# Kernel tuning notes

Hardware: AMD Instinct MI355X
Metric: run time of the kernel (lower is better)

The kernel has to match this reference:

```python
import jax, jax.numpy as jnp
import numpy as np
import math

N_HEADS = 16
KV_HEADS = 4
HEAD_DIM = 128
ROPE_BASE = 1000000.0


def _make_rope(seq_len, dim, base=ROPE_BASE):
    inv_freq = 1.0 / (base ** (np.arange(0, dim, 2, dtype=np.float32) / dim))
    t = np.arange(seq_len, dtype=np.float32)
    freqs = np.outer(t, inv_freq)                     # [S, dim/2]
    emb = np.concatenate([freqs, freqs], axis=-1)     # [S, dim]
    return jnp.asarray(np.cos(emb)), jnp.asarray(np.sin(emb))


def setup_inputs() -> dict:
    key = jax.random.key(0)
    ks = jax.random.split(key, 6)
    B, S, H = 2, 2048, 2048
    kv_dim = KV_HEADS * HEAD_DIM
    s = 1.0 / math.sqrt(H)
    x = jax.random.normal(ks[0], (B, S, H), jnp.float32)
    wq = jax.random.normal(ks[1], (H, H), jnp.float32) * s
    wk = jax.random.normal(ks[2], (kv_dim, H), jnp.float32) * s
    wv = jax.random.normal(ks[3], (kv_dim, H), jnp.float32) * s
    wo = jax.random.normal(ks[4], (H, H), jnp.float32) * s
    bq = jnp.zeros((H,), jnp.float32)
    bk = jnp.zeros((kv_dim,), jnp.float32)
    bv = jnp.zeros((kv_dim,), jnp.float32)
    bo = jnp.zeros((H,), jnp.float32)
    cos, sin = _make_rope(S, HEAD_DIM)
    return {"x": x, "wq": wq, "bq": bq, "wk": wk, "bk": bk,
            "wv": wv, "bv": bv, "wo": wo, "bo": bo, "cos": cos, "sin": sin}


def _rotate_half(t):
    half = t.shape[-1] // 2
    return jnp.concatenate([-t[..., half:], t[..., :half]], axis=-1)


def reference(x, wq, bq, wk, bk, wv, bv, wo, bo, cos, sin):
    B, S, H = x.shape
    hd, nh, kvh = HEAD_DIM, N_HEADS, KV_HEADS
    rep = nh // kvh

    q = (x @ wq.T + bq).reshape(B, S, nh, hd)
    k = (x @ wk.T + bk).reshape(B, S, kvh, hd)
    v = (x @ wv.T + bv).reshape(B, S, kvh, hd)

    # RoPE (rotate-half), cos/sin: [S, hd] -> broadcast over batch and heads
    c = cos[None, :, None, :]
    s_ = sin[None, :, None, :]
    q = q * c + _rotate_half(q) * s_
    k = k * c + _rotate_half(k) * s_

    # GQA: expand KV heads by rep
    k = jnp.repeat(k, rep, axis=2)   # [B, S, nh, hd]
    v = jnp.repeat(v, rep, axis=2)

    q = q.transpose(0, 2, 1, 3)      # [B, nh, S, hd]
    k = k.transpose(0, 2, 1, 3)
    v = v.transpose(0, 2, 1, 3)

    score = jnp.einsum('bhqd,bhkd->bhqk', q, k) / math.sqrt(hd)
    causal = jnp.triu(jnp.full((S, S), -jnp.inf, jnp.float32), k=1)
    score = score + causal
    attn = jax.nn.softmax(score.astype(jnp.float32), axis=-1).astype(q.dtype)

    out = jnp.einsum('bhqk,bhkd->bhqd', attn, v)   # [B, nh, S, hd]
    out = out.transpose(0, 2, 1, 3).reshape(B, S, nh * hd)
    return out @ wo.T + bo
```

## Files before the change

### kernel.cpp

```cpp
#include <hip/hip_runtime.h>

typedef unsigned short u16;
typedef __bf16 bf16x8 __attribute__((ext_vector_type(8)));
typedef float  f32x4  __attribute__((ext_vector_type(4)));

#define SEQ 2048

__device__ __forceinline__ float bf2f(u16 u) {
    union { unsigned int i; float f; } c;
    c.i = ((unsigned int)u) << 16;
    return c.f;
}
__device__ __forceinline__ u16 f2bf(float f) {
    union { float f; unsigned int i; } c;
    c.f = f;
    unsigned int u = c.i;
    u += 0x7FFFu + ((u >> 16) & 1u);
    return (u16)(u >> 16);
}

__device__ __forceinline__ void gl_lds16(const u16* g, u16* l) {
    __builtin_amdgcn_global_load_lds(
        (const __attribute__((address_space(1))) unsigned int*)(g),
        (__attribute__((address_space(3))) unsigned int*)(l), 16, 0, 0);
}

__device__ __forceinline__ void cvt4(const float* s, u16* d) {
    float4 v = *(const float4*)s;
    ushort4 o;
    o.x = f2bf(v.x); o.y = f2bf(v.y); o.z = f2bf(v.z); o.w = f2bf(v.w);
    *(ushort4*)d = o;
}

__global__ void prep(const float* __restrict__ x,
                     const float* __restrict__ wq, const float* __restrict__ wk,
                     const float* __restrict__ wv,
                     const float* __restrict__ bq, const float* __restrict__ bk,
                     const float* __restrict__ bv,
                     u16* __restrict__ xb, u16* __restrict__ wqkvb,
                     float* __restrict__ biasb)
{
    const int E0 = 2097152;
    const int E1 = E0 + 1048576;
    const int E2 = E1 + 262144;
    const int E3 = E2 + 262144;
    const int E4 = E3 + 768;
    int i = blockIdx.x * blockDim.x + threadIdx.x;
    int stride = gridDim.x * blockDim.x;
    for (; i < E4; i += stride) {
        if (i < E0)      cvt4(x  + (size_t)i * 4,        xb    + (size_t)i * 4);
        else if (i < E1) cvt4(wq + (size_t)(i - E0) * 4, wqkvb + (size_t)(i - E0) * 4);
        else if (i < E2) cvt4(wk + (size_t)(i - E1) * 4, wqkvb + 4194304 + (size_t)(i - E1) * 4);
        else if (i < E3) cvt4(wv + (size_t)(i - E2) * 4, wqkvb + 5242880 + (size_t)(i - E2) * 4);
        else {
            int j = i - E3;
            const float* src = (j < 512) ? (bq + j * 4)
                             : (j < 640) ? (bk + (j - 512) * 4)
                                         : (bv + (j - 640) * 4);
            *(float4*)&biasb[j * 4] = *(const float4*)src;
        }
    }
}

__global__ void cvt_f32_bf16(const float* __restrict__ in, u16* __restrict__ out, int n4) {
    int i = blockIdx.x * blockDim.x + threadIdx.x;
    int stride = gridDim.x * blockDim.x;
    for (; i < n4; i += stride) cvt4(in + (size_t)i * 4, out + (size_t)i * 4);
}

template<int MODE>
__global__ __launch_bounds__(256) void gemm_bt(
    const u16* __restrict__ A, const u16* __restrict__ B,
    const float* __restrict__ bias, float* __restrict__ C,
    u16* __restrict__ qb, u16* __restrict__ kb, u16* __restrict__ vt,
    int M, int N, int K)
{
    __shared__ __align__(16) u16 lA[128 * 32];
    __shared__ __align__(16) u16 lB[128 * 32];
    const int tid   = threadIdx.x;
    const int lane  = tid & 63;
    const int wave  = tid >> 6;
    const int waveM = (wave >> 1) * 64;
    const int waveN = (wave & 1) * 64;
    const int bm = blockIdx.x * 128;
    const int bn = blockIdx.y * 128;
    const int lrow = lane & 15;
    const int koff = (lane >> 4) * 8;

    f32x4 acc[4][4] = {};

    for (int k0 = 0; k0 < K; k0 += 32) {
        __syncthreads();
#pragma unroll
        for (int p = 0; p < 2; ++p) {
            int idx = p * 256 + tid;
            int row = idx >> 2;
            int ch  = idx & 3;
            gl_lds16(&A[(size_t)(bm + row) * K + k0 + ch * 8], &lA[(p * 256 + wave * 64) * 8]);
            gl_lds16(&B[(size_t)(bn + row) * K + k0 + ch * 8], &lB[(p * 256 + wave * 64) * 8]);
        }
        __syncthreads();

        bf16x8 af[4], bfr[4];
#pragma unroll
        for (int i = 0; i < 4; ++i)
            af[i] = *(const bf16x8*)&lA[(waveM + i * 16 + lrow) * 32 + koff];
#pragma unroll
        for (int j = 0; j < 4; ++j)
            bfr[j] = *(const bf16x8*)&lB[(waveN + j * 16 + lrow) * 32 + koff];
#pragma unroll
        for (int i = 0; i < 4; ++i)
#pragma unroll
            for (int j = 0; j < 4; ++j)
                acc[i][j] = __builtin_amdgcn_mfma_f32_16x16x32_bf16(
                    af[i], bfr[j], acc[i][j], 0, 0, 0);
    }

    const int r4 = (lane >> 4) * 4;
    const int cn = lane & 15;
#pragma unroll
    for (int i = 0; i < 4; ++i) {
#pragma unroll
        for (int j = 0; j < 4; ++j) {
            int row0 = bm + waveM + i * 16 + r4;
            int col  = bn + waveN + j * 16 + cn;
            float bc = bias[col];
#pragma unroll
            for (int r = 0; r < 4; ++r) {
                float val = acc[i][j][r] + bc;
                if (MODE == 0) {
                    C[(size_t)(row0 + r) * N + col] = val;
                } else {
                    int row = row0 + r;
                    int b = row >> 11;
                    int s = row & 2047;
                    int d = col & 127;
                    u16 o = f2bf(val);
                    if (col < 2048) {
                        int h = col >> 7;
                        qb[(((size_t)(b * 16 + h) * SEQ) + s) * 128 + d] = o;
                    } else if (col < 2560) {
                        int h = (col - 2048) >> 7;
                        kb[(((size_t)(b * 4 + h) * SEQ) + s) * 128 + d] = o;
                    } else {
                        int h = (col - 2560) >> 7;
                        vt[(((size_t)(b * 4 + h) * 128) + d) * SEQ + s] = o;
                    }
                }
            }
        }
    }
}

__global__ void rope_k(u16* __restrict__ kb,
                       const float* __restrict__ cosb, const float* __restrict__ sinb)
{
    const int n = 16384 * 64;
    int i = blockIdx.x * blockDim.x + threadIdx.x;
    if (i >= n) return;
    int d0  = i & 63;
    int row = i >> 6;
    u16* base = kb + (size_t)row * 128;
    int s = row & (SEQ - 1);
    float c  = cosb[s * 128 + d0];
    float sn = sinb[s * 128 + d0];
    float a0 = bf2f(base[d0]);
    float a1 = bf2f(base[d0 + 64]);
    base[d0]      = f2bf(a0 * c - a1 * sn);
    base[d0 + 64] = f2bf(a1 * c + a0 * sn);
}

__global__ __launch_bounds__(256, 2) void attn_mfma(
    const u16* __restrict__ qb, const u16* __restrict__ kb,
    const u16* __restrict__ vt, u16* __restrict__ ob,
    const float* __restrict__ cosb, const float* __restrict__ sinb)
{
    __shared__ __align__(16) u16 Ks[2][4][64][32];
    __shared__ __align__(16) u16 Vts[2][2][128][32];
    __shared__ __align__(16) u16 Ph[4][16][64];

    const int id   = blockIdx.x;
    const int s8   = id & 7;
    const int n    = id >> 3;
    const int pair = n & 15;
    const int h_lo = n >> 4;
    const int b    = s8 >> 2;
    const int kvh  = s8 & 3;
    const int h    = kvh * 4 + h_lo;
    const int qA   = pair, qB = 31 - pair;

    const int tid  = threadIdx.x;
    const int lane = tid & 63;
    const int w    = tid >> 6;
    const int c16  = lane & 15;
    const int quad = lane >> 4;
    const int T    = w >> 1;
    const int sub  = w & 1;
    const int qT   = T ? qB : qA;
    const float qscale = 0.08838834764831845f * 1.4426950408889634f;

    const u16* kbase  = kb + ((size_t)(b * 4 + kvh) * SEQ) * 128;
    const u16* vtbase = vt + ((size_t)(b * 4 + kvh) * 128) * SEQ;

    bf16x8 qf[2][4];
#pragma unroll
    for (int s = 0; s < 2; ++s) {
        const int spos = qT * 64 + sub * 32 + s * 16 + c16;
        const u16* qp = qb + (((size_t)(b * 16 + h)) * SEQ + spos) * 128;
        bf16x8 t[4];
#pragma unroll
        for (int kk = 0; kk < 4; ++kk)
            t[kk] = *(const bf16x8*)(qp + kk * 32 + quad * 8);
#pragma unroll
        for (int kk = 0; kk < 2; ++kk) {
            const float* cp = cosb + (size_t)spos * 128 + kk * 32 + quad * 8;
            const float* sp = sinb + (size_t)spos * 128 + kk * 32 + quad * 8;
#pragma unroll
            for (int e = 0; e < 8; ++e) {
                float a0 = (float)t[kk][e];
                float a1 = (float)t[kk + 2][e];
                float c  = cp[e];
                float sn = sp[e];
                qf[s][kk][e]     = (__bf16)((a0 * c - a1 * sn) * qscale);
                qf[s][kk + 2][e] = (__bf16)((a1 * c + a0 * sn) * qscale);
            }
        }
    }

    int ksrc[4], vsrc[4];
#pragma unroll
    for (int it = 0; it < 4; ++it) {
        int o  = (it * 4 + w) * 1024 + lane * 16;
        int kk = o >> 12;
        int r  = (o >> 6) & 63;
        int c  = (o >> 4) & 3;
        ksrc[it] = r * 128 + kk * 32 + c * 8;
        int p2 = o >> 13;
        int d  = (o >> 6) & 127;
        vsrc[it] = d * SEQ + p2 * 32 + c * 8;
    }

    const int nB = qB + 1;
    const int rowL0 = qT * 64 + sub * 32 + quad * 4;

    f32x4 o[2][8] = {};
    float l[2][4] = {};

    u16* KsF  = &Ks[0][0][0][0];
    u16* VtsF = &Vts[0][0][0][0];

#pragma unroll
    for (int it = 0; it < 4; ++it) {
        gl_lds16(kbase  + ksrc[it], KsF  + (it * 4 + w) * 512);
        gl_lds16(vtbase + vsrc[it], VtsF + (it * 4 + w) * 512);
    }
    __syncthreads();

    for (int kt = 0; kt < nB; ++kt) {
        const int cur = kt & 1;

        if (kt + 1 < nB) {
            const u16* kg = kbase  + (size_t)(kt + 1) * (64 * 128);
            const u16* vg = vtbase + (kt + 1) * 64;
            u16* kd = KsF  + ((kt + 1) & 1) * (4 * 64 * 32);
            u16* vd = VtsF + ((kt + 1) & 1) * (2 * 128 * 32);
#pragma unroll
            for (int it = 0; it < 4; ++it) {
                gl_lds16(kg + ksrc[it], kd + (it * 4 + w) * 512);
                gl_lds16(vg + vsrc[it], vd + (it * 4 + w) * 512);
            }
        }

        if (T == 1 || kt <= qA) {
            f32x4 sS[2][4] = {};
#pragma unroll
            for (int kk = 0; kk < 4; ++kk)
#pragma unroll
                for (int j = 0; j < 4; ++j) {
                    bf16x8 kf = *(const bf16x8*)&Ks[cur][kk][j * 16 + c16][quad * 8];
                    sS[0][j] = __builtin_amdgcn_mfma_f32_16x16x32_bf16(qf[0][kk], kf, sS[0][j], 0, 0, 0);
                    sS[1][j] = __builtin_amdgcn_mfma_f32_16x16x32_bf16(qf[1][kk], kf, sS[1][j], 0, 0, 0);
                }

            if (kt == qT) {
#pragma unroll
                for (int s = 0; s < 2; ++s)
#pragma unroll
                    for (int j = 0; j < 4; ++j)
#pragma unroll
                        for (int rr = 0; rr < 4; ++rr)
                            if (kt * 64 + j * 16 + c16 > rowL0 + s * 16 + rr) sS[s][j][rr] = -1e30f;
            }

            bf16x8 pa[2][2];
#pragma unroll
            for (int s = 0; s < 2; ++s) {
#pragma unroll
                for (int jj = 0; jj < 4; ++jj)
#pragma unroll
                    for (int rr = 0; rr < 4; ++rr) {
                        float p = __builtin_amdgcn_exp2f(sS[s][jj][rr]);
                        l[s][rr] += p;
                        int row = quad * 4 + rr;
                        *(__bf16*)&Ph[w][row][(((jj * 2 + (c16 >> 3)) + row) & 7) * 8 + (c16 & 7)] = (__bf16)p;
                    }
#pragma unroll
                for (int k2 = 0; k2 < 2; ++k2)
                    pa[s][k2] = *(const bf16x8*)&Ph[w][c16][(((k2 * 4 + quad) + c16) & 7) * 8];
            }

#pragma unroll
            for (int k2 = 0; k2 < 2; ++k2)
#pragma unroll
                for (int nt = 0; nt < 8; ++nt) {
                    bf16x8 vf = *(const bf16x8*)&Vts[cur][k2][nt * 16 + c16][quad * 8];
                    o[0][nt] = __builtin_amdgcn_mfma_f32_16x16x32_bf16(pa[0][k2], vf, o[0][nt], 0, 0, 0);
                    o[1][nt] = __builtin_amdgcn_mfma_f32_16x16x32_bf16(pa[1][k2], vf, o[1][nt], 0, 0, 0);
                }
        }

        __syncthreads();
    }

#pragma unroll
    for (int s = 0; s < 2; ++s) {
        float li[4];
#pragma unroll
        for (int rr = 0; rr < 4; ++rr) {
            float la = l[s][rr];
            la += __shfl_xor(la, 1);
            la += __shfl_xor(la, 2);
            la += __shfl_xor(la, 4);
            la += __shfl_xor(la, 8);
            li[rr] = 1.0f / la;
        }
        const size_t rowG = (size_t)b * SEQ + rowL0 + s * 16;
#pragma unroll
        for (int nt = 0; nt < 8; ++nt)
#pragma unroll
            for (int rr = 0; rr < 4; ++rr)
                ob[(rowG + rr) * 2048 + h * 128 + nt * 16 + c16] = f2bf(o[s][nt][rr] * li[rr]);
    }
}

extern "C" void kernel_launch(void* const* d_in, const int* in_sizes, int n_in,
                              void* d_out, int out_size, void* d_ws, size_t ws_size,
                              hipStream_t stream) {
    const float* x    = (const float*)d_in[0];
    const float* wq   = (const float*)d_in[1];
    const float* bq   = (const float*)d_in[2];
    const float* wk   = (const float*)d_in[3];
    const float* bk   = (const float*)d_in[4];
    const float* wv   = (const float*)d_in[5];
    const float* bv   = (const float*)d_in[6];
    const float* wo   = (const float*)d_in[7];
    const float* bo   = (const float*)d_in[8];
    const float* cosb = (const float*)d_in[9];
    const float* sinb = (const float*)d_in[10];
    float* out = (float*)d_out;

    char* ws = (char*)d_ws;
    const size_t OFF_WQKV = 0;
    const size_t OFF_BIAS = 12582912;
    const size_t OFF_QB   = 12599296;
    const size_t OFF_KB   = 29376512;
    const size_t OFF_VT   = 33570816;
    const size_t OFF_XB   = 37765120;

    u16*   wqkvb = (u16*)(ws + OFF_WQKV);
    u16*   wob   = (u16*)(ws + OFF_WQKV);
    float* biasb = (float*)(ws + OFF_BIAS);
    u16*   qb2   = (u16*)(ws + OFF_QB);
    u16*   kb2   = (u16*)(ws + OFF_KB);
    u16*   vt2   = (u16*)(ws + OFF_VT);
    u16*   xb    = (u16*)(ws + OFF_XB);
    u16*   attnb = (u16*)(ws + OFF_XB);

    prep<<<4096, 256, 0, stream>>>(x, wq, wk, wv, bq, bk, bv, xb, wqkvb, biasb);

    gemm_bt<1><<<dim3(32, 24), 256, 0, stream>>>(xb, wqkvb, biasb, nullptr,
                                                 qb2, kb2, vt2, 4096, 3072, 2048);

    cvt_f32_bf16<<<4096, 256, 0, stream>>>(wo, wob, 1048576);

    rope_k<<<4096, 256, 0, stream>>>(kb2, cosb, sinb);

    attn_mfma<<<512, 256, 0, stream>>>(qb2, kb2, vt2, attnb, cosb, sinb);

    gemm_bt<0><<<dim3(32, 16), 256, 0, stream>>>(attnb, wob, bo, out,
                                                 nullptr, nullptr, nullptr, 4096, 2048, 2048);
}
```

Baseline: 342.4 us.

## Use K=64 tiled QKV GEMM and fold Wo conversion into prep kernel

Adds a gemm_bt64 variant that stages 64-wide K slices in LDS with an XOR swizzle and issues two MFMA k-steps per barrier pair. This halves the number of sync and load rounds for the QKV projection. When the workspace is large enough, the Wo fp32-to-bf16 conversion also moves into the prep kernel at a separate offset, which removes one launch. The cost is doubled LDS use per block, which may lower occupancy, and a fallback path that depends on workspace size.

```diff
diff --git a/kernel.cpp b/kernel.cpp
--- a/kernel.cpp
+++ b/kernel.cpp
@@ -34,30 +34,34 @@
 
 __global__ void prep(const float* __restrict__ x,
                      const float* __restrict__ wq, const float* __restrict__ wk,
-                     const float* __restrict__ wv,
+                     const float* __restrict__ wv, const float* __restrict__ wo,
                      const float* __restrict__ bq, const float* __restrict__ bk,
                      const float* __restrict__ bv,
                      u16* __restrict__ xb, u16* __restrict__ wqkvb,
-                     float* __restrict__ biasb)
+                     float* __restrict__ biasb, u16* __restrict__ wob)
 {
     const int E0 = 2097152;
     const int E1 = E0 + 1048576;
     const int E2 = E1 + 262144;
     const int E3 = E2 + 262144;
     const int E4 = E3 + 768;
+    const int EN = wob ? (E4 + 1048576) : E4;
     int i = blockIdx.x * blockDim.x + threadIdx.x;
     int stride = gridDim.x * blockDim.x;
-    for (; i < E4; i += stride) {
+    for (; i < EN; i += stride) {
         if (i < E0)      cvt4(x  + (size_t)i * 4,        xb    + (size_t)i * 4);
         else if (i < E1) cvt4(wq + (size_t)(i - E0) * 4, wqkvb + (size_t)(i - E0) * 4);
         else if (i < E2) cvt4(wk + (size_t)(i - E1) * 4, wqkvb + 4194304 + (size_t)(i - E1) * 4);
         else if (i < E3) cvt4(wv + (size_t)(i - E2) * 4, wqkvb + 5242880 + (size_t)(i - E2) * 4);
-        else {
+        else if (i < E4) {
             int j = i - E3;
             const float* src = (j < 512) ? (bq + j * 4)
                              : (j < 640) ? (bk + (j - 512) * 4)
                                          : (bv + (j - 640) * 4);
             *(float4*)&biasb[j * 4] = *(const float4*)src;
+        } else {
+            int j = i - E4;
+            cvt4(wo + (size_t)j * 4, wob + (size_t)j * 4);
         }
     }
 }
@@ -152,6 +156,100 @@
     }
 }
 
+template<int MODE>
+__global__ __launch_bounds__(256) void gemm_bt64(
+    const u16* __restrict__ A, const u16* __restrict__ B,
+    const float* __restrict__ bias, float* __restrict__ C,
+    u16* __restrict__ qb, u16* __restrict__ kb, u16* __restrict__ vt,
+    int M, int N, int K)
+{
+    __shared__ __align__(16) u16 lA[128 * 64];
+    __shared__ __align__(16) u16 lB[128 * 64];
+    const int tid   = threadIdx.x;
+    const int lane  = tid & 63;
+    const int wave  = tid >> 6;
+    const int waveM = (wave >> 1) * 64;
+    const int waveN = (wave & 1) * 64;
+    const int bm = blockIdx.x * 128;
+    const int bn = blockIdx.y * 128;
+    const int lrow = lane & 15;
+    const int quad = lane >> 4;
+
+    int srow[4], scol[4];
+#pragma unroll
+    for (int it = 0; it < 4; ++it) {
+        int Lc  = it * 256 + tid;
+        int row = Lc >> 3;
+        srow[it] = row;
+        scol[it] = ((Lc & 7) ^ (row & 7)) * 8;
+    }
+
+    f32x4 acc[4][4] = {};
+
+    for (int k0 = 0; k0 < K; k0 += 64) {
+        __syncthreads();
+#pragma unroll
+        for (int it = 0; it < 4; ++it) {
+            gl_lds16(&A[(size_t)(bm + srow[it]) * K + k0 + scol[it]], &lA[(it * 4 + wave) * 512]);
+            gl_lds16(&B[(size_t)(bn + srow[it]) * K + k0 + scol[it]], &lB[(it * 4 + wave) * 512]);
+        }
+        __syncthreads();
+
+#pragma unroll
+        for (int kk = 0; kk < 2; ++kk) {
+            bf16x8 af[4], bfr[4];
+            const int xr = (kk * 4 + quad) ^ (lrow & 7);
+#pragma unroll
+            for (int i = 0; i < 4; ++i)
+                af[i] = *(const bf16x8*)&lA[(waveM + i * 16 + lrow) * 64 + xr * 8];
+#pragma unroll
+            for (int j = 0; j < 4; ++j)
+                bfr[j] = *(const bf16x8*)&lB[(waveN + j * 16 + lrow) * 64 + xr * 8];
+#pragma unroll
+            for (int i = 0; i < 4; ++i)
+#pragma unroll
+                for (int j = 0; j < 4; ++j)
+                    acc[i][j] = __builtin_amdgcn_mfma_f32_16x16x32_bf16(
+                        af[i], bfr[j], acc[i][j], 0, 0, 0);
+        }
+    }
+
+    const int r4 = quad * 4;
+    const int cn = lrow;
+#pragma unroll
+    for (int i = 0; i < 4; ++i) {
+#pragma unroll
+        for (int j = 0; j < 4; ++j) {
+            int row0 = bm + waveM + i * 16 + r4;
+            int col  = bn + waveN + j * 16 + cn;
+            float bc = bias[col];
+#pragma unroll
+            for (int r = 0; r < 4; ++r) {
+                float val = acc[i][j][r] + bc;
+                if (MODE == 0) {
+                    C[(size_t)(row0 + r) * N + col] = val;
+                } else {
+                    int row = row0 + r;
+                    int b = row >> 11;
+                    int s = row & 2047;
+                    int d = col & 127;
+                    u16 o = f2bf(val);
+                    if (col < 2048) {
+                        int h = col >> 7;
+                        qb[(((size_t)(b * 16 + h) * SEQ) + s) * 128 + d] = o;
+                    } else if (col < 2560) {
+                        int h = (col - 2048) >> 7;
+                        kb[(((size_t)(b * 4 + h) * SEQ) + s) * 128 + d] = o;
+                    } else {
+                        int h = (col - 2560) >> 7;
+                        vt[(((size_t)(b * 4 + h) * 128) + d) * SEQ + s] = o;
+                    }
+                }
+            }
+        }
+    }
+}
+
 __global__ void rope_k(u16* __restrict__ kb,
                        const float* __restrict__ cosb, const float* __restrict__ sinb)
 {
@@ -366,22 +464,26 @@
     const size_t OFF_KB   = 29376512;
     const size_t OFF_VT   = 33570816;
     const size_t OFF_XB   = 37765120;
+    const size_t OFF_WOB  = 54542336;
+    const bool bigws = ws_size >= (OFF_WOB + 8388608);
 
     u16*   wqkvb = (u16*)(ws + OFF_WQKV);
-    u16*   wob   = (u16*)(ws + OFF_WQKV);
     float* biasb = (float*)(ws + OFF_BIAS);
     u16*   qb2   = (u16*)(ws + OFF_QB);
     u16*   kb2   = (u16*)(ws + OFF_KB);
     u16*   vt2   = (u16*)(ws + OFF_VT);
     u16*   xb    = (u16*)(ws + OFF_XB);
     u16*   attnb = (u16*)(ws + OFF_XB);
-
-    prep<<<4096, 256, 0, stream>>>(x, wq, wk, wv, bq, bk, bv, xb, wqkvb, biasb);
-
-    gemm_bt<1><<<dim3(32, 24), 256, 0, stream>>>(xb, wqkvb, biasb, nullptr,
-                                                 qb2, kb2, vt2, 4096, 3072, 2048);
-
-    cvt_f32_bf16<<<4096, 256, 0, stream>>>(wo, wob, 1048576);
+    u16*   wob   = bigws ? (u16*)(ws + OFF_WOB)
+                         : (u16*)(ws + OFF_WQKV);
+
+    prep<<<4096, 256, 0, stream>>>(x, wq, wk, wv, wo, bq, bk, bv,
+                                   xb, wqkvb, biasb, bigws ? wob : nullptr);
+
+    gemm_bt64<1><<<dim3(32, 24), 256, 0, stream>>>(xb, wqkvb, biasb, nullptr,
+                                                   qb2, kb2, vt2, 4096, 3072, 2048);
+
+    if (!bigws) cvt_f32_bf16<<<4096, 256, 0, stream>>>(wo, wob, 1048576);
 
     rope_k<<<4096, 256, 0, stream>>>(kb2, cosb, sinb);
 
```

Result: slower. 352.0 us (+2.8%).
